# Performance work log

Measured on AMD Instinct MI355X. Metric: run time of the kernel, lower is better.

## Reference

```python
import jax, jax.numpy as jnp
import numpy as np

SIGMA = 0.2
BN_EPS = 1e-5


def setup_inputs() -> dict:
    key = jax.random.key(0)
    k1, k2, k3, k4 = jax.random.split(key, 4)
    B, N, K = 8, 16384, 64
    normals = jax.random.normal(k1, (B, 3, N), dtype=jnp.float32)
    # normalize to unit normals (faithful to what the module consumes in practice)
    normals = normals / jnp.linalg.norm(normals, axis=1, keepdims=True)
    neighbor_idx = jax.random.randint(k2, (B, N, 3), 0, N, dtype=jnp.int64)
    weight_alpha = jax.random.uniform(k3, (1, K, 4), dtype=jnp.float32) * np.pi
    weight_beta = jax.random.uniform(k4, (1, K, 4), dtype=jnp.float32) * (2 * np.pi)
    bn_gamma = jnp.ones((K,), dtype=jnp.float32)
    bn_beta = jnp.zeros((K,), dtype=jnp.float32)
    return {
        "normals": normals,
        "neighbor_idx": neighbor_idx,
        "weight_alpha": weight_alpha,
        "weight_beta": weight_beta,
        "bn_gamma": bn_gamma,
        "bn_beta": bn_beta,
    }


def reference(normals, neighbor_idx, weight_alpha, weight_beta, bn_gamma, bn_beta):
    # normals: (B, 3, N); neighbor_idx: (B, N, 3)
    # kernel directions on unit sphere: W[c, k, m], c in xyz, m in 4 points per kernel
    W = jnp.concatenate(
        [
            jnp.sin(weight_alpha) * jnp.cos(weight_beta),
            jnp.sin(weight_alpha) * jnp.sin(weight_beta),
            jnp.cos(weight_alpha),
        ],
        axis=0,
    )  # (3, K, 4)

    # gather neighbor normals: nbr[b, c, i, j] = normals[b, c, neighbor_idx[b, i, j]]
    nbr = jax.vmap(lambda nm, idx: nm[:, idx])(normals, neighbor_idx)  # (B, 3, N, 3)
    F = jnp.concatenate([normals[:, :, :, None], nbr], axis=3)  # (B, 3, N, 4) face points p

    # squared distances via ||f||^2 + ||w||^2 - 2 f.w  (avoids 6D broadcast of torch code)
    dots = jnp.einsum("bcnp,ckm->bknpm", F, W)  # (B, K, N, 4, 4)
    F2 = jnp.sum(F * F, axis=1)[:, None, :, :, None]  # (B, 1, N, 4, 1)
    W2 = jnp.sum(W * W, axis=0)[None, :, None, None, :]  # (1, K, 1, 1, 4)
    dist = F2 + W2 - 2.0 * dots  # (B, K, N, 4, 4)

    inv = -1.0 / (2.0 * SIGMA * SIGMA)
    feat = jnp.sum(jnp.exp(dist * inv), axis=(3, 4)) / 16.0  # (B, K, N)

    # BatchNorm1d (training mode, biased variance over batch+spatial dims) + ReLU
    mean = jnp.mean(feat, axis=(0, 2), keepdims=True)
    var = jnp.var(feat, axis=(0, 2), keepdims=True)
    xhat = (feat - mean) * jax.lax.rsqrt(var + BN_EPS)
    out = bn_gamma[None, :, None] * xhat + bn_beta[None, :, None]
    return jax.nn.relu(out)
```

## Files before the change

### kernel.cpp

```cpp
#include <hip/hip_runtime.h>

#define BB 8
#define NN 16384
#define KK 64
#define GRID_FUSED 2048

#if __has_builtin(__builtin_amdgcn_exp2f)
#define EXP2(x) __builtin_amdgcn_exp2f(x)
#else
#define EXP2(x) exp2f(x)
#endif

typedef float v2f __attribute__((ext_vector_type(2)));

#if __has_builtin(__builtin_elementwise_fma)
#define FMA2(a, b, c) __builtin_elementwise_fma((a), (b), (c))
#else
static __device__ inline v2f FMA2(v2f a, v2f b, v2f c) {
    v2f r; r.x = fmaf(a.x, b.x, c.x); r.y = fmaf(a.y, b.y, c.y); return r;
}
#endif

#define LOG2E 1.44269504088896340736f
#define CW (25.0f * LOG2E)
#define CE (-12.5f * LOG2E)
#define BN_EPS_SCALED 2.56e-3f

__global__ __launch_bounds__(256) void fkc_prep(
    const float* __restrict__ walpha, const float* __restrict__ wbeta,
    float* __restrict__ wx, float* __restrict__ wy, float* __restrict__ wz,
    float* __restrict__ gsum, float* __restrict__ gss,
    unsigned* __restrict__ bar)
{
    const int t = threadIdx.x;
    if (t < 64) { gsum[t] = 0.0f; gss[t] = 0.0f; }
    if (t == 64) { *bar = 0u; }
    float a = walpha[t];
    float b = wbeta[t];
    float sa = __sinf(a);
    wx[t] = CW * sa * __cosf(b);
    wy[t] = CW * sa * __sinf(b);
    wz[t] = CW * __cosf(a);
}

__global__ __launch_bounds__(256, 8) void fkc_fused(
    const float* __restrict__ normals,
    const int*   __restrict__ nidx,
    const float* __restrict__ wx, const float* __restrict__ wy,
    const float* __restrict__ wz,
    float* __restrict__ out,
    float* __restrict__ gsum,
    float* __restrict__ gss,
    const float* __restrict__ gamma,
    const float* __restrict__ beta,
    unsigned* __restrict__ bar)
{
    __shared__ float fl[16][257];
    __shared__ float ps[16][17], pq[16][17];
    __shared__ float scs[16], shs[16];

    const int tid = threadIdx.x;
    const int pg = blockIdx.x >> 2;
    const int k0 = (blockIdx.x & 3) * 16;
    const int gid = pg * 256 + tid;
    const int b = gid >> 14;
    const int n = gid & (NN - 1);
    const float* nb = normals + b * 3 * NN;

    float fx[4], fy[4], fz[4];
    fx[0] = nb[n];
    fy[0] = nb[NN + n];
    fz[0] = nb[2 * NN + n];
    const int ibase = (b * NN + n) * 3;
#pragma unroll
    for (int j = 0; j < 3; ++j) {
        int id = nidx[ibase + j];
        fx[j + 1] = nb[id];
        fy[j + 1] = nb[NN + id];
        fz[j + 1] = nb[2 * NN + id];
    }

    v2f fx01 = {fx[0], fx[1]}, fx23 = {fx[2], fx[3]};
    v2f fy01 = {fy[0], fy[1]}, fy23 = {fy[2], fy[3]};
    v2f fz01 = {fz[0], fz[1]}, fz23 = {fz[2], fz[3]};
    v2f e01, e23;
    {
        v2f n2a = FMA2(fx01, fx01, FMA2(fy01, fy01, fz01 * fz01));
        v2f n2b = FMA2(fx23, fx23, FMA2(fy23, fy23, fz23 * fz23));
        e01 = CE * (n2a + 1.0f);
        e23 = CE * (n2b + 1.0f);
    }

#pragma unroll
    for (int kk = 0; kk < 16; ++kk) {
        v2f acc01 = {0.0f, 0.0f}, acc23 = {0.0f, 0.0f};
#pragma unroll
        for (int m = 0; m < 4; ++m) {
            const int wi = ((k0 + kk) << 2) + m;
            float wxv = wx[wi], wyv = wy[wi], wzv = wz[wi];
            v2f wx2 = {wxv, wxv}, wy2 = {wyv, wyv}, wz2 = {wzv, wzv};
            v2f a01 = FMA2(fz01, wz2, FMA2(fy01, wy2, FMA2(fx01, wx2, e01)));
            v2f a23 = FMA2(fz23, wz2, FMA2(fy23, wy2, FMA2(fx23, wx2, e23)));
            v2f x01 = {EXP2(a01.x), EXP2(a01.y)};
            v2f x23 = {EXP2(a23.x), EXP2(a23.y)};
            acc01 += x01;
            acc23 += x23;
        }
        v2f t2 = acc01 + acc23;
        fl[kk][tid] = t2.x + t2.y;
    }
    __syncthreads();

    {
        const int k = tid & 15;
        const int part = tid >> 4;
        float s = 0.0f, ss = 0.0f;
#pragma unroll
        for (int r = 0; r < 16; ++r) {
            float v = fl[k][part * 16 + r];
            s += v;
            ss = fmaf(v, v, ss);
        }
        ps[k][part] = s;
        pq[k][part] = ss;
    }
    __syncthreads();

    if (tid < 16) {
        float s = 0.0f;
#pragma unroll
        for (int r = 0; r < 16; ++r) s += ps[tid][r];
        atomicAdd(&gsum[k0 + tid], s);
    } else if (tid < 32) {
        const int kk = tid - 16;
        float ss = 0.0f;
#pragma unroll
        for (int r = 0; r < 16; ++r) ss += pq[kk][r];
        atomicAdd(&gss[k0 + kk], ss);
    }

    __syncthreads();
    if (tid == 0) {
        __hip_atomic_fetch_add(bar, 1u, __ATOMIC_RELEASE,
                               __HIP_MEMORY_SCOPE_AGENT);
        int polls = 0;
        while (__hip_atomic_load(bar, __ATOMIC_RELAXED,
                                 __HIP_MEMORY_SCOPE_AGENT) < GRID_FUSED) {
            __builtin_amdgcn_s_sleep(64);
            if (++polls > 30000) break;
        }
        __threadfence();
    }
    __syncthreads();

    if (tid < 16) {
        const float invM = 1.0f / (float)(BB * NN);
        float s = __hip_atomic_load(&gsum[k0 + tid], __ATOMIC_RELAXED,
                                    __HIP_MEMORY_SCOPE_AGENT);
        float q = __hip_atomic_load(&gss[k0 + tid], __ATOMIC_RELAXED,
                                    __HIP_MEMORY_SCOPE_AGENT);
        float mean = s * invM;
        float var = fmaf(-mean, mean, q * invM);
        float sc = gamma[k0 + tid] * rsqrtf(var + BN_EPS_SCALED);
        scs[tid] = sc;
        shs[tid] = fmaf(-mean, sc, beta[k0 + tid]);
    }
    __syncthreads();

    float* orow = out + (b * KK + k0) * NN + n;
#pragma unroll
    for (int kk = 0; kk < 16; ++kk) {
        orow[kk * NN] = fmaxf(fmaf(fl[kk][tid], scs[kk], shs[kk]), 0.0f);
    }
}

__global__ __launch_bounds__(256, 8) void fkc_main(
    const float* __restrict__ normals, const int* __restrict__ nidx,
    const float* __restrict__ wx, const float* __restrict__ wy,
    const float* __restrict__ wz,
    float* __restrict__ out, float* __restrict__ gsum, float* __restrict__ gss)
{
    __shared__ float fl[16][257];
    __shared__ float ps[16][17], pq[16][17];

    const int tid = threadIdx.x;
    const int pg = blockIdx.x >> 2;
    const int k0 = (blockIdx.x & 3) * 16;
    const int gid = pg * 256 + tid;
    const int b = gid >> 14;
    const int n = gid & (NN - 1);
    const float* nb = normals + b * 3 * NN;

    float fx[4], fy[4], fz[4];
    fx[0] = nb[n];
    fy[0] = nb[NN + n];
    fz[0] = nb[2 * NN + n];
    const int ibase = (b * NN + n) * 3;
#pragma unroll
    for (int j = 0; j < 3; ++j) {
        int id = nidx[ibase + j];
        fx[j + 1] = nb[id];
        fy[j + 1] = nb[NN + id];
        fz[j + 1] = nb[2 * NN + id];
    }

    v2f fx01 = {fx[0], fx[1]}, fx23 = {fx[2], fx[3]};
    v2f fy01 = {fy[0], fy[1]}, fy23 = {fy[2], fy[3]};
    v2f fz01 = {fz[0], fz[1]}, fz23 = {fz[2], fz[3]};
    v2f e01, e23;
    {
        v2f n2a = FMA2(fx01, fx01, FMA2(fy01, fy01, fz01 * fz01));
        v2f n2b = FMA2(fx23, fx23, FMA2(fy23, fy23, fz23 * fz23));
        e01 = CE * (n2a + 1.0f);
        e23 = CE * (n2b + 1.0f);
    }

    float* orow = out + (b * KK + k0) * NN + n;
#pragma unroll
    for (int kk = 0; kk < 16; ++kk) {
        v2f acc01 = {0.0f, 0.0f}, acc23 = {0.0f, 0.0f};
#pragma unroll
        for (int m = 0; m < 4; ++m) {
            const int wi = ((k0 + kk) << 2) + m;
            float wxv = wx[wi], wyv = wy[wi], wzv = wz[wi];
            v2f wx2 = {wxv, wxv}, wy2 = {wyv, wyv}, wz2 = {wzv, wzv};
            v2f a01 = FMA2(fz01, wz2, FMA2(fy01, wy2, FMA2(fx01, wx2, e01)));
            v2f a23 = FMA2(fz23, wz2, FMA2(fy23, wy2, FMA2(fx23, wx2, e23)));
            v2f x01 = {EXP2(a01.x), EXP2(a01.y)};
            v2f x23 = {EXP2(a23.x), EXP2(a23.y)};
            acc01 += x01;
            acc23 += x23;
        }
        v2f t2 = acc01 + acc23;
        float acc = t2.x + t2.y;
        orow[kk * NN] = acc;
        fl[kk][tid] = acc;
    }
    __syncthreads();

    {
        const int k = tid & 15;
        const int part = tid >> 4;
        float s = 0.0f, ss = 0.0f;
#pragma unroll
        for (int r = 0; r < 16; ++r) {
            float v = fl[k][part * 16 + r];
            s += v;
            ss = fmaf(v, v, ss);
        }
        ps[k][part] = s;
        pq[k][part] = ss;
    }
    __syncthreads();

    if (tid < 16) {
        float s = 0.0f;
#pragma unroll
        for (int r = 0; r < 16; ++r) s += ps[tid][r];
        atomicAdd(&gsum[k0 + tid], s);
    } else if (tid < 32) {
        const int kk = tid - 16;
        float ss = 0.0f;
#pragma unroll
        for (int r = 0; r < 16; ++r) ss += pq[kk][r];
        atomicAdd(&gss[k0 + kk], ss);
    }
}

__global__ __launch_bounds__(256) void fkc_apply(
    float4* __restrict__ out4,
    const float* __restrict__ gsum, const float* __restrict__ gss,
    const float* __restrict__ gamma, const float* __restrict__ beta)
{
    const int i = blockIdx.x * 256 + threadIdx.x;
    const int k = (i >> 12) & (KK - 1);

    const float invM = 1.0f / (float)(BB * NN);
    float mean = gsum[k] * invM;
    float var = fmaf(-mean, mean, gss[k] * invM);
    float sc = gamma[k] * rsqrtf(var + BN_EPS_SCALED);
    float sh = fmaf(-mean, sc, beta[k]);

    float4 v = out4[i];
    v.x = fmaxf(fmaf(v.x, sc, sh), 0.0f);
    v.y = fmaxf(fmaf(v.y, sc, sh), 0.0f);
    v.z = fmaxf(fmaf(v.z, sc, sh), 0.0f);
    v.w = fmaxf(fmaf(v.w, sc, sh), 0.0f);
    out4[i] = v;
}

extern "C" void kernel_launch(void* const* d_in, const int* in_sizes, int n_in,
                              void* d_out, int out_size, void* d_ws, size_t ws_size,
                              hipStream_t stream) {
    const float* normals = (const float*)d_in[0];
    const int*   nidx    = (const int*)d_in[1];
    const float* walpha  = (const float*)d_in[2];
    const float* wbeta   = (const float*)d_in[3];
    const float* gamma   = (const float*)d_in[4];
    const float* beta    = (const float*)d_in[5];
    float* out = (float*)d_out;
    float* ws = (float*)d_ws;

    float* gsum   = ws;
    float* gss    = ws + 64;
    unsigned* bar = (unsigned*)(ws + 128);
    float* wxb    = ws + 192;
    float* wyb    = ws + 448;
    float* wzb    = ws + 704;

    static int use_fused = -1;
    if (use_fused < 0) {
        int occ = 0, ncu = 0, dev = 0;
        hipError_t e1 = hipOccupancyMaxActiveBlocksPerMultiprocessor(
            &occ, fkc_fused, 256, 0);
        hipGetDevice(&dev);
        hipError_t e2 = hipDeviceGetAttribute(
            &ncu, hipDeviceAttributeMultiprocessorCount, dev);
        use_fused = (e1 == hipSuccess && e2 == hipSuccess &&
                     (long)occ * ncu >= GRID_FUSED) ? 1 : 0;
    }

    fkc_prep<<<1, 256, 0, stream>>>(walpha, wbeta, wxb, wyb, wzb,
                                    gsum, gss, bar);
    if (use_fused) {
        fkc_fused<<<GRID_FUSED, 256, 0, stream>>>(
            normals, nidx, wxb, wyb, wzb, out, gsum, gss, gamma, beta, bar);
    } else {
        fkc_main<<<2048, 256, 0, stream>>>(normals, nidx, wxb, wyb, wzb,
                                           out, gsum, gss);
        fkc_apply<<<8192, 256, 0, stream>>>((float4*)out, gsum, gss,
                                            gamma, beta);
    }
}
```

Measured before the change: 108.6 us.

## Replace global grid barrier with per-channel-group hierarchical tree barrier

Swaps the single global arrival counter for a two-level tree barrier. Blocks for each 16-channel group count into eight padded sub-counters, then a root counter, and the last arrival sets per-sub release flags. Blocks now wait only for the other blocks that add to the same channel statistics, and spinning is spread across separate cache lines, which aims to cut atomic contention and barrier latency. It also removes the release ordering and thread fence and relies on relaxed atomics only, which weakens the guarantee that the statistic sums are visible when read.

Measured after the change: 109.0 us. Within noise of the previous version (+0.4%).

```diff
diff --git a/kernel.cpp b/kernel.cpp
--- a/kernel.cpp
+++ b/kernel.cpp
@@ -26,42 +26,47 @@
 #define CE (-12.5f * LOG2E)
 #define BN_EPS_SCALED 2.56e-3f
 
+#define WS_SUB 128
+#define WS_ROOT 640
+#define WS_FLAG 704
+#define WS_WX 1216
+
 __global__ __launch_bounds__(256) void fkc_prep(
     const float* __restrict__ walpha, const float* __restrict__ wbeta,
-    float* __restrict__ wx, float* __restrict__ wy, float* __restrict__ wz,
-    float* __restrict__ gsum, float* __restrict__ gss,
-    unsigned* __restrict__ bar)
+    float* __restrict__ ws)
 {
     const int t = threadIdx.x;
-    if (t < 64) { gsum[t] = 0.0f; gss[t] = 0.0f; }
-    if (t == 64) { *bar = 0u; }
+    for (int i = t; i < WS_WX; i += 256) ws[i] = 0.0f;
     float a = walpha[t];
     float b = wbeta[t];
     float sa = __sinf(a);
-    wx[t] = CW * sa * __cosf(b);
-    wy[t] = CW * sa * __sinf(b);
-    wz[t] = CW * __cosf(a);
+    ws[WS_WX + t]       = CW * sa * __cosf(b);
+    ws[WS_WX + 256 + t] = CW * sa * __sinf(b);
+    ws[WS_WX + 512 + t] = CW * __cosf(a);
 }
 
 __global__ __launch_bounds__(256, 8) void fkc_fused(
     const float* __restrict__ normals,
     const int*   __restrict__ nidx,
-    const float* __restrict__ wx, const float* __restrict__ wy,
-    const float* __restrict__ wz,
+    float* __restrict__ ws,
     float* __restrict__ out,
-    float* __restrict__ gsum,
-    float* __restrict__ gss,
     const float* __restrict__ gamma,
-    const float* __restrict__ beta,
-    unsigned* __restrict__ bar)
+    const float* __restrict__ beta)
 {
     __shared__ float fl[16][257];
     __shared__ float ps[16][17], pq[16][17];
     __shared__ float scs[16], shs[16];
 
+    const float* wx = ws + WS_WX;
+    const float* wy = ws + WS_WX + 256;
+    const float* wz = ws + WS_WX + 512;
+    float* gsum = ws;
+    float* gss  = ws + 64;
+
     const int tid = threadIdx.x;
     const int pg = blockIdx.x >> 2;
-    const int k0 = (blockIdx.x & 3) * 16;
+    const int q  = blockIdx.x & 3;
+    const int k0 = q * 16;
     const int gid = pg * 256 + tid;
     const int b = gid >> 14;
     const int n = gid & (NN - 1);
@@ -140,16 +145,34 @@
     }
 
     __syncthreads();
+
     if (tid == 0) {
-        __hip_atomic_fetch_add(bar, 1u, __ATOMIC_RELEASE,
-                               __HIP_MEMORY_SCOPE_AGENT);
+        const int j = pg & 7;
+        unsigned* sub  = (unsigned*)(ws + WS_SUB)  + (q * 8 + j) * 16;
+        unsigned* root = (unsigned*)(ws + WS_ROOT) + q * 16;
+        unsigned* flg  = (unsigned*)(ws + WS_FLAG) + (q * 8 + j) * 16;
+
+        unsigned old = __hip_atomic_fetch_add(sub, 1u, __ATOMIC_RELAXED,
+                                              __HIP_MEMORY_SCOPE_AGENT);
+        if (old == 63u) {
+            unsigned r = __hip_atomic_fetch_add(root, 1u, __ATOMIC_RELAXED,
+                                                __HIP_MEMORY_SCOPE_AGENT);
+            if (r == 7u) {
+#pragma unroll
+                for (int jj = 0; jj < 8; ++jj) {
+                    unsigned* f = (unsigned*)(ws + WS_FLAG) + (q * 8 + jj) * 16;
+                    __hip_atomic_store(f, 1u, __ATOMIC_RELAXED,
+                                       __HIP_MEMORY_SCOPE_AGENT);
+                }
+            }
+        }
         int polls = 0;
-        while (__hip_atomic_load(bar, __ATOMIC_RELAXED,
-                                 __HIP_MEMORY_SCOPE_AGENT) < GRID_FUSED) {
-            __builtin_amdgcn_s_sleep(64);
-            if (++polls > 30000) break;
-        }
-        __threadfence();
+        while (__hip_atomic_load(flg, __ATOMIC_RELAXED,
+                                 __HIP_MEMORY_SCOPE_AGENT) == 0u) {
+            __builtin_amdgcn_s_sleep(32);
+            if (++polls > 150000) break;
+        }
+        __asm__ __volatile__("" ::: "memory");
     }
     __syncthreads();
 
@@ -157,10 +180,10 @@
         const float invM = 1.0f / (float)(BB * NN);
         float s = __hip_atomic_load(&gsum[k0 + tid], __ATOMIC_RELAXED,
                                     __HIP_MEMORY_SCOPE_AGENT);
-        float q = __hip_atomic_load(&gss[k0 + tid], __ATOMIC_RELAXED,
-                                    __HIP_MEMORY_SCOPE_AGENT);
+        float qq = __hip_atomic_load(&gss[k0 + tid], __ATOMIC_RELAXED,
+                                     __HIP_MEMORY_SCOPE_AGENT);
         float mean = s * invM;
-        float var = fmaf(-mean, mean, q * invM);
+        float var = fmaf(-mean, mean, qq * invM);
         float sc = gamma[k0 + tid] * rsqrtf(var + BN_EPS_SCALED);
         scs[tid] = sc;
         shs[tid] = fmaf(-mean, sc, beta[k0 + tid]);
@@ -176,12 +199,17 @@
 
 __global__ __launch_bounds__(256, 8) void fkc_main(
     const float* __restrict__ normals, const int* __restrict__ nidx,
-    const float* __restrict__ wx, const float* __restrict__ wy,
-    const float* __restrict__ wz,
-    float* __restrict__ out, float* __restrict__ gsum, float* __restrict__ gss)
+    float* __restrict__ ws,
+    float* __restrict__ out)
 {
     __shared__ float fl[16][257];
     __shared__ float ps[16][17], pq[16][17];
+
+    const float* wx = ws + WS_WX;
+    const float* wy = ws + WS_WX + 256;
+    const float* wz = ws + WS_WX + 512;
+    float* gsum = ws;
+    float* gss  = ws + 64;
 
     const int tid = threadIdx.x;
     const int pg = blockIdx.x >> 2;
@@ -269,15 +297,15 @@
 
 __global__ __launch_bounds__(256) void fkc_apply(
     float4* __restrict__ out4,
-    const float* __restrict__ gsum, const float* __restrict__ gss,
+    const float* __restrict__ ws,
     const float* __restrict__ gamma, const float* __restrict__ beta)
 {
     const int i = blockIdx.x * 256 + threadIdx.x;
     const int k = (i >> 12) & (KK - 1);
 
     const float invM = 1.0f / (float)(BB * NN);
-    float mean = gsum[k] * invM;
-    float var = fmaf(-mean, mean, gss[k] * invM);
+    float mean = ws[k] * invM;
+    float var = fmaf(-mean, mean, ws[64 + k] * invM);
     float sc = gamma[k] * rsqrtf(var + BN_EPS_SCALED);
     float sh = fmaf(-mean, sc, beta[k]);
 
@@ -301,13 +329,6 @@
     float* out = (float*)d_out;
     float* ws = (float*)d_ws;
 
-    float* gsum   = ws;
-    float* gss    = ws + 64;
-    unsigned* bar = (unsigned*)(ws + 128);
-    float* wxb    = ws + 192;
-    float* wyb    = ws + 448;
-    float* wzb    = ws + 704;
-
     static int use_fused = -1;
     if (use_fused < 0) {
         int occ = 0, ncu = 0, dev = 0;
@@ -320,15 +341,12 @@
                      (long)occ * ncu >= GRID_FUSED) ? 1 : 0;
     }
 
-    fkc_prep<<<1, 256, 0, stream>>>(walpha, wbeta, wxb, wyb, wzb,
-                                    gsum, gss, bar);
+    fkc_prep<<<1, 256, 0, stream>>>(walpha, wbeta, ws);
     if (use_fused) {
         fkc_fused<<<GRID_FUSED, 256, 0, stream>>>(
-            normals, nidx, wxb, wyb, wzb, out, gsum, gss, gamma, beta, bar);
+            normals, nidx, ws, out, gamma, beta);
     } else {
-        fkc_main<<<2048, 256, 0, stream>>>(normals, nidx, wxb, wyb, wzb,
-                                           out, gsum, gss);
-        fkc_apply<<<8192, 256, 0, stream>>>((float4*)out, gsum, gss,
-                                            gamma, beta);
-    }
-}
+        fkc_main<<<2048, 256, 0, stream>>>(normals, nidx, ws, out);
+        fkc_apply<<<8192, 256, 0, stream>>>((float4*)out, ws, gamma, beta);
+    }
+}
```
